# Optimization experiments

Measured on AMD Instinct MI355X. Metric: run time of the kernel, lower is better.

The kernel has to match this reference:

```python
import jax, jax.numpy as jnp
import numpy as np

# Architecture constants (from init_kwargs / Mamba2 defaults)
NL = 4          # num_layer per direction
DM = 256        # d_model (attention_in)
DS = 128        # d_state
DC = 4          # d_conv
DI = 2 * DM     # d_inner = expand * d_model = 512
HD = 64         # headdim
NH = DI // HD   # nheads = 8
NG = 1          # ngroups
D_XBC = DI + 2 * NG * DS           # 768 conv channels
D_INP = 2 * DI + 2 * NG * DS + NH  # 1288 in_proj width
EPS = 1e-5


def rmsnorm(x, w):
    return x * jax.lax.rsqrt(jnp.mean(x * x, axis=-1, keepdims=True) + EPS) * w


def causal_dwconv(x, w, b):
    # x: (B, L, C); w: (C, K); b: (C,) -- causal depthwise conv
    K = w.shape[1]
    L = x.shape[1]
    xp = jnp.pad(x, ((0, 0), (K - 1, 0), (0, 0)))
    y = b
    for k in range(K):  # K=4, fixed small kernel
        y = y + xp[:, k:k + L, :] * w[:, k]
    return y


def ssd_scan(xh, dt, A_log, Bm, Cm):
    # xh: (B,L,H,P), dt: (B,L,H), A_log: (H,), Bm/Cm: (B,L,N) (ngroups=1, broadcast over heads)
    A = -jnp.exp(A_log)                 # (H,)
    decay = jnp.exp(dt * A)             # (B,L,H)
    dtx = dt[..., None] * xh            # (B,L,H,P)
    B, L, H, P = xh.shape
    N = Bm.shape[-1]

    def step(h, inp):
        dec, u, bt, ct = inp            # (B,H), (B,H,P), (B,N), (B,N)
        h = h * dec[..., None, None] + u[..., None] * bt[:, None, None, :]
        y = jnp.einsum('bhpn,bn->bhp', h, ct)
        return h, y

    h0 = jnp.zeros((B, H, P, N), xh.dtype)
    xs = (jnp.moveaxis(decay, 1, 0), jnp.moveaxis(dtx, 1, 0),
          jnp.moveaxis(Bm, 1, 0), jnp.moveaxis(Cm, 1, 0))
    _, ys = jax.lax.scan(step, h0, xs)  # ys: (L,B,H,P)
    return jnp.moveaxis(ys, 0, 1)


def mamba2_mixer(u, Wi, cw, cb, dtb, Al, Dp, gw, Wo):
    B, L, _ = u.shape
    zxbcdt = u @ Wi                                   # (B,L,1288)
    z = zxbcdt[..., :DI]
    xBC = zxbcdt[..., DI:DI + D_XBC]
    dt = zxbcdt[..., DI + D_XBC:]
    xBC = jax.nn.silu(causal_dwconv(xBC, cw, cb))
    xh = xBC[..., :DI].reshape(B, L, NH, HD)
    Bm = xBC[..., DI:DI + NG * DS]
    Cm = xBC[..., DI + NG * DS:]
    dt = jax.nn.softplus(dt + dtb)                    # (B,L,H)
    y = ssd_scan(xh, dt, Al, Bm, Cm) + xh * Dp[None, None, :, None]
    y = y.reshape(B, L, DI)
    g = rmsnorm(y * jax.nn.silu(z), gw)               # RMSNormGated
    return g @ Wo


def run_stack(x, block_ids, nw, Wi, cw, cb, dtb, Al, Dp, gw, Wo):
    res = None
    h = x
    for i in block_ids:
        res = h + res if res is not None else h
        h = mamba2_mixer(rmsnorm(res, nw[i]), Wi[i], cw[i], cb[i],
                         dtb[i], Al[i], Dp[i], gw[i], Wo[i])
    return h + res


def setup_inputs() -> dict:
    key = jax.random.key(0)
    ks = jax.random.split(key, 8)
    B, L = 4, 2048
    NB = 2 * NL  # 8 blocks: forward + backward
    x = jax.random.normal(ks[0], (B, L, DM), jnp.float32)
    nw = jnp.ones((NB, DM), jnp.float32)
    Wi = jax.random.normal(ks[1], (NB, DM, D_INP), jnp.float32) * 0.02
    cw = jax.random.normal(ks[2], (NB, D_XBC, DC), jnp.float32) * 0.2
    cb = jnp.zeros((NB, D_XBC), jnp.float32)
    dt0 = jax.random.uniform(ks[3], (NB, NH), jnp.float32, 0.001, 0.1)
    dtb = dt0 + jnp.log(-jnp.expm1(-dt0))  # inverse softplus
    Al = jnp.log(jax.random.uniform(ks[4], (NB, NH), jnp.float32, 1.0, 16.0))
    Dp = jnp.ones((NB, NH), jnp.float32)
    gw = jnp.ones((NB, DI), jnp.float32)
    Wo = jax.random.normal(ks[5], (NB, DI, DM), jnp.float32) * 0.02
    return {"x": x, "block_norm_w": nw, "in_proj_w": Wi, "conv_w": cw,
            "conv_b": cb, "dt_bias": dtb, "A_log": Al, "D": Dp,
            "gnorm_w": gw, "out_proj_w": Wo}


def reference(x, block_norm_w, in_proj_w, conv_w, conv_b, dt_bias, A_log, D, gnorm_w, out_proj_w):
    fwd = run_stack(x, range(NL), block_norm_w, in_proj_w, conv_w, conv_b,
                    dt_bias, A_log, D, gnorm_w, out_proj_w)
    bwd = run_stack(jnp.flip(x, 1), range(NL, 2 * NL), block_norm_w, in_proj_w,
                    conv_w, conv_b, dt_bias, A_log, D, gnorm_w, out_proj_w)
    return fwd + jnp.flip(bwd, 1)  # bidirectional_merging='add'
```

## Files before the change

### kernel.cpp

```cpp
#include <hip/hip_runtime.h>
#include <hip/hip_bf16.h>
#include <math.h>

#define LSEQ 2048
#define BREAL 4
#define BT 8
#define DM 256
#define DI 512
#define DSZ 128
#define NHEADS 8
#define HDIM 64
#define DXBC 768
#define DINP 1288
#define NINP_PAD 1408
#define NLAYERS 4
#define QCH 64
#define NCH (LSEQ/QCH)
#define CTL 64
#define EPSF 1e-5f

typedef __attribute__((ext_vector_type(8))) short short8b;
typedef __attribute__((ext_vector_type(4))) float f32x4;

__device__ __forceinline__ float siluf(float x){ return x / (1.f + __expf(-x)); }
__device__ __forceinline__ unsigned short f2bf(float x){
    union { float f; unsigned u; } c; c.f = x;
    unsigned r = (c.u + 0x7FFFu + ((c.u >> 16) & 1u)) >> 16;
    return (unsigned short)r;
}
__device__ __forceinline__ float bf2f(unsigned short u){
    union { unsigned u; float f; } c; c.u = ((unsigned)u) << 16;
    return c.f;
}

__global__ __launch_bounds__(256) void k_prep(const float* __restrict__ x, float* __restrict__ res){
    int i = blockIdx.x*256 + threadIdx.x;
    int d4 = i & (DM/4 - 1);
    int t  = i >> 6;
    int l  = t % LSEQ;
    int b  = t / LSEQ;
    const float4* x4 = (const float4*)x;
    float4 v;
    if (b < BREAL) v = x4[((size_t)(b*LSEQ) + l)*(DM/4) + d4];
    else           v = x4[((size_t)((b-BREAL)*LSEQ) + (LSEQ-1-l))*(DM/4) + d4];
    ((float4*)res)[i] = v;
}

__global__ __launch_bounds__(256) void k_wtrans(const float* __restrict__ W, unsigned short* __restrict__ WT,
                                                int K, int N, int Npad){
    __shared__ float sT[32][33];
    int n0 = blockIdx.x*32, k0 = blockIdx.y*32, g = blockIdx.z;
    const float* Wg = W + (size_t)g*K*N;
    unsigned short* WTg = WT + (size_t)g*Npad*K;
    int t = threadIdx.x;
    int r = t >> 3, c4 = (t & 7)*4;
    float4 v;
    if (n0 + c4 + 3 < N) v = *(const float4*)(Wg + (size_t)(k0+r)*N + n0 + c4);
    else {
        float tmp[4];
        #pragma unroll
        for (int j = 0; j < 4; j++) tmp[j] = (n0 + c4 + j < N) ? Wg[(size_t)(k0+r)*N + n0 + c4 + j] : 0.f;
        v = make_float4(tmp[0],tmp[1],tmp[2],tmp[3]);
    }
    sT[c4+0][r] = v.x; sT[c4+1][r] = v.y; sT[c4+2][r] = v.z; sT[c4+3][r] = v.w;
    __syncthreads();
    ushort4 o;
    o.x = f2bf(sT[r][c4+0]); o.y = f2bf(sT[r][c4+1]); o.z = f2bf(sT[r][c4+2]); o.w = f2bf(sT[r][c4+3]);
    *(ushort4*)(WTg + (size_t)(n0+r)*K + k0 + c4) = o;
}

__global__ __launch_bounds__(256) void k_resnorm(const float* __restrict__ res,
                                                 const float* __restrict__ nw, int li,
                                                 unsigned short* __restrict__ u){
    int wid  = (blockIdx.x*256 + threadIdx.x) >> 6;
    int lane = threadIdx.x & 63;
    int b = wid / LSEQ;
    const float* rr = res + (size_t)wid*DM;
    float4 v = ((const float4*)rr)[lane];
    float ss = v.x*v.x + v.y*v.y + v.z*v.z + v.w*v.w;
    #pragma unroll
    for (int o = 32; o >= 1; o >>= 1) ss += __shfl_xor(ss, o, 64);
    float sc = rsqrtf(ss*(1.f/DM) + EPSF);
    int blk = (b < BREAL) ? li : li + NLAYERS;
    float4 w = ((const float4*)(nw + (size_t)blk*DM))[lane];
    ushort4 o4;
    o4.x = f2bf(v.x*sc*w.x); o4.y = f2bf(v.y*sc*w.y); o4.z = f2bf(v.z*sc*w.z); o4.w = f2bf(v.w*sc*w.w);
    *(ushort4*)(u + (size_t)wid*DM + lane*4) = o4;
}

__global__ __launch_bounds__(256) void k_gemm_mfma(const unsigned short* __restrict__ A,
                                                   const unsigned short* __restrict__ WT,
                                                   int K, int N, size_t wt_group_stride, int rows_per_group,
                                                   float* __restrict__ Cf, unsigned short* __restrict__ Cb,
                                                   int mode){
    __shared__ unsigned short sA[128][40];
    __shared__ unsigned short sW[128][40];
    int bn = blockIdx.x, bm = blockIdx.y;
    int row0 = bm*128, n0 = bn*128;
    const unsigned short* WTg = WT + (size_t)(row0 / rows_per_group) * wt_group_stride;
    int t = threadIdx.x;
    int w = t >> 6, lane = t & 63;
    int wr = w >> 1, wc = w & 1;
    int l15 = lane & 15, lg = lane >> 4;
    f32x4 acc[4][4];
    #pragma unroll
    for (int mi = 0; mi < 4; mi++)
        #pragma unroll
        for (int ni = 0; ni < 4; ni++) acc[mi][ni] = (f32x4){0.f,0.f,0.f,0.f};

    int srow = t >> 1, shalf = t & 1;
    const unsigned short* Ap = A + (size_t)(row0 + srow)*K + shalf*16;
    const unsigned short* Wp = WTg + (size_t)(n0 + srow)*K + shalf*16;

    for (int k0 = 0; k0 < K; k0 += 32){
        int4 a0 = *(const int4*)(Ap + k0);
        int4 a1 = *(const int4*)(Ap + k0 + 8);
        int4 w0 = *(const int4*)(Wp + k0);
        int4 w1 = *(const int4*)(Wp + k0 + 8);
        __syncthreads();
        *(int4*)&sA[srow][shalf*16]     = a0;
        *(int4*)&sA[srow][shalf*16 + 8] = a1;
        *(int4*)&sW[srow][shalf*16]     = w0;
        *(int4*)&sW[srow][shalf*16 + 8] = w1;
        __syncthreads();
        short8b af[4], bf[4];
        #pragma unroll
        for (int mi = 0; mi < 4; mi++) af[mi] = *(const short8b*)&sA[wr*64 + mi*16 + l15][lg*8];
        #pragma unroll
        for (int ni = 0; ni < 4; ni++) bf[ni] = *(const short8b*)&sW[wc*64 + ni*16 + l15][lg*8];
        #pragma unroll
        for (int mi = 0; mi < 4; mi++)
            #pragma unroll
            for (int ni = 0; ni < 4; ni++)
                acc[mi][ni] = __builtin_amdgcn_mfma_f32_16x16x32_bf16(af[mi], bf[ni], acc[mi][ni], 0, 0, 0);
    }
    #pragma unroll
    for (int mi = 0; mi < 4; mi++)
        #pragma unroll
        for (int ni = 0; ni < 4; ni++){
            int col = n0 + wc*64 + ni*16 + l15;
            if (col < N){
                #pragma unroll
                for (int r = 0; r < 4; r++){
                    int row = row0 + wr*64 + mi*16 + lg*4 + r;
                    if (mode == 1)      Cb[(size_t)row*N + col] = f2bf(acc[mi][ni][r]);
                    else if (mode == 2) Cf[(size_t)row*N + col] += acc[mi][ni][r];
                    else                Cf[(size_t)row*N + col] = acc[mi][ni][r];
                }
            }
        }
}

__global__ __launch_bounds__(256) void k_conv2(const unsigned short* __restrict__ zxb,
                                               const float* __restrict__ cw, const float* __restrict__ cb,
                                               const float* __restrict__ dtb, const float* __restrict__ Al,
                                               int li, unsigned short* __restrict__ xbcb,
                                               float* __restrict__ dtO, float* __restrict__ laO){
    int bid = blockIdx.x;
    int ch = bid % 3;
    int tl = (bid/3) % (LSEQ/CTL);
    int b  = bid / (3*(LSEQ/CTL));
    int c  = ch*256 + threadIdx.x;
    int blk = (b < BREAL) ? li : li + NLAYERS;
    float4 wv = *(const float4*)(cw + (size_t)blk*DXBC*4 + c*4);
    float bias = cb[(size_t)blk*DXBC + c];
    int l0 = tl*CTL;
    size_t base = ((size_t)b*LSEQ)*DINP + DI + c;
    float xm3 = (l0 >= 3) ? bf2f(zxb[base + (size_t)(l0-3)*DINP]) : 0.f;
    float xm2 = (l0 >= 2) ? bf2f(zxb[base + (size_t)(l0-2)*DINP]) : 0.f;
    float xm1 = (l0 >= 1) ? bf2f(zxb[base + (size_t)(l0-1)*DINP]) : 0.f;
    for (int l = l0; l < l0 + CTL; l++){
        float xv = bf2f(zxb[base + (size_t)l*DINP]);
        float acc = bias + xm3*wv.x + xm2*wv.y + xm1*wv.z + xv*wv.w;
        xbcb[((size_t)(b*LSEQ)+l)*DXBC + c] = f2bf(siluf(acc));
        xm3 = xm2; xm2 = xm1; xm1 = xv;
    }
    if (ch == 0){
        #pragma unroll
        for (int it = 0; it < 2; it++){
            int e = threadIdx.x*2 + it;
            int h = e & 7, dl = e >> 3;
            size_t bl = (size_t)b*LSEQ + l0 + dl;
            float raw = bf2f(zxb[bl*DINP + DI + DXBC + h]) + dtb[blk*NHEADS + h];
            float d = (raw > 20.f) ? raw : log1pf(__expf(raw));
            dtO[bl*NHEADS + h] = d;
            laO[bl*NHEADS + h] = -d*__expf(Al[blk*NHEADS + h]);
        }
    }
}

__global__ __launch_bounds__(256) void k_chunk_state(const unsigned short* __restrict__ xbcb,
                                                     const float* __restrict__ dt, const float* __restrict__ la,
                                                     unsigned short* __restrict__ states, float* __restrict__ decp){
    __shared__ unsigned short sBT[DSZ][72];
    __shared__ unsigned short sXT[HDIM][72];
    __shared__ float sW[4][QCH];
    int bid = blockIdx.x;
    int hg = bid & 1;
    int c  = (bid >> 1) & (NCH-1);
    int b  = bid >> 6;
    int t = threadIdx.x;
    int w = t >> 6, lane = t & 63, l15 = lane & 15, lg = lane >> 4;
    size_t bl0 = (size_t)b*LSEQ + c*QCH;

    {
        int h = hg*4 + w;
        float v = la[(bl0 + lane)*NHEADS + h];
        #pragma unroll
        for (int o = 1; o < 64; o <<= 1){
            float u = __shfl_up(v, o, 64);
            if (lane >= o) v += u;
        }
        float saQ = __shfl(v, 63, 64);
        float dtv = dt[(bl0 + lane)*NHEADS + h];
        sW[w][lane] = dtv * __expf(saQ - v);
        if (lane == 63) decp[((size_t)b*NHEADS + h)*NCH + c] = __expf(v);
    }
    #pragma unroll
    for (int it = 0; it < 4; it++){
        int e = t + 256*it;
        int j = e >> 4, n8 = (e & 15)*8;
        int4 v = *(const int4*)(xbcb + (bl0 + j)*DXBC + DI + n8);
        const unsigned short* pv = (const unsigned short*)&v;
        #pragma unroll
        for (int i = 0; i < 8; i++) sBT[n8+i][j] = pv[i];
    }
    __syncthreads();

    int p0 = (w >> 1)*32, n0 = (w & 1)*64;
    for (int hh = 0; hh < 4; hh++){
        int h = hg*4 + hh;
        #pragma unroll
        for (int it = 0; it < 4; it++){
            int e = t + 256*it;
            int j = e >> 4, p4 = (e & 15)*4;
            ushort4 v = *(const ushort4*)(xbcb + (bl0 + j)*DXBC + h*HDIM + p4);
            float s = sW[hh][j];
            sXT[p4+0][j] = f2bf(bf2f(v.x)*s);
            sXT[p4+1][j] = f2bf(bf2f(v.y)*s);
            sXT[p4+2][j] = f2bf(bf2f(v.z)*s);
            sXT[p4+3][j] = f2bf(bf2f(v.w)*s);
        }
        __syncthreads();
        f32x4 acc[2][4];
        #pragma unroll
        for (int mi = 0; mi < 2; mi++)
            #pragma unroll
            for (int ni = 0; ni < 4; ni++) acc[mi][ni] = (f32x4){0.f,0.f,0.f,0.f};
        #pragma unroll
        for (int kk = 0; kk < 2; kk++){
            short8b a[2], bb[4];
            #pragma unroll
            for (int mi = 0; mi < 2; mi++) a[mi]  = *(const short8b*)&sXT[p0 + mi*16 + l15][kk*32 + lg*8];
            #pragma unroll
            for (int ni = 0; ni < 4; ni++) bb[ni] = *(const short8b*)&sBT[n0 + ni*16 + l15][kk*32 + lg*8];
            #pragma unroll
            for (int mi = 0; mi < 2; mi++)
                #pragma unroll
                for (int ni = 0; ni < 4; ni++)
                    acc[mi][ni] = __builtin_amdgcn_mfma_f32_16x16x32_bf16(a[mi], bb[ni], acc[mi][ni], 0, 0, 0);
        }
        unsigned short* sp = states + (((size_t)b*NHEADS + h)*NCH + c)*(HDIM*DSZ);
        #pragma unroll
        for (int mi = 0; mi < 2; mi++)
            #pragma unroll
            for (int ni = 0; ni < 4; ni++)
                #pragma unroll
                for (int r = 0; r < 4; r++){
                    int p = p0 + mi*16 + lg*4 + r;
                    int n = n0 + ni*16 + l15;
                    sp[(size_t)p*DSZ + n] = f2bf(acc[mi][ni][r]);
                }
        __syncthreads();
    }
}

__global__ __launch_bounds__(256) void k_scan2(unsigned short* __restrict__ states, const float* __restrict__ decp){
    int bh = blockIdx.x >> 3, slice = blockIdx.x & 7;
    int t = threadIdx.x;
    size_t base = (size_t)bh*NCH*(HDIM*DSZ) + slice*1024 + t*4;
    float H0=0.f, H1=0.f, H2=0.f, H3=0.f;
    for (int c = 0; c < NCH; c++){
        float P = decp[bh*NCH + c];
        unsigned short* sp = states + base + (size_t)c*(HDIM*DSZ);
        ushort4 S = *(ushort4*)sp;
        ushort4 Hw;
        Hw.x = f2bf(H0); Hw.y = f2bf(H1); Hw.z = f2bf(H2); Hw.w = f2bf(H3);
        *(ushort4*)sp = Hw;
        H0 = fmaf(H0, P, bf2f(S.x));
        H1 = fmaf(H1, P, bf2f(S.y));
        H2 = fmaf(H2, P, bf2f(S.z));
        H3 = fmaf(H3, P, bf2f(S.w));
    }
}

__global__ __launch_bounds__(256) void k_chunk_y(const unsigned short* __restrict__ xbcb,
                                                 const float* __restrict__ dt, const float* __restrict__ la,
                                                 const unsigned short* __restrict__ states,
                                                 const float* __restrict__ Dp, int li,
                                                 unsigned short* __restrict__ y){
    __shared__ unsigned short sB_[QCH][136];
    __shared__ unsigned short sC_[QCH][136];
    __shared__ unsigned short sS[QCH][72];
    __shared__ unsigned short sXT[HDIM][72];
    __shared__ unsigned short sH[HDIM][136];
    __shared__ float sSa[4][QCH];
    __shared__ float sDt[4][QCH];
    int bid = blockIdx.x;
    int hg = bid & 1;
    int c  = (bid >> 1) & (NCH-1);
    int b  = bid >> 6;
    int blk = (b < BREAL) ? li : li + NLAYERS;
    int t = threadIdx.x;
    int w = t >> 6, lane = t & 63, l15 = lane & 15, lg = lane >> 4;
    size_t bl0 = (size_t)b*LSEQ + c*QCH;

    {
        int h = hg*4 + w;
        float v = la[(bl0 + lane)*NHEADS + h];
        #pragma unroll
        for (int o = 1; o < 64; o <<= 1){
            float u = __shfl_up(v, o, 64);
            if (lane >= o) v += u;
        }
        sSa[w][lane] = v;
        sDt[w][lane] = dt[(bl0 + lane)*NHEADS + h];
    }
    #pragma unroll
    for (int it = 0; it < 4; it++){
        int e = t + 256*it;
        int j = e >> 4, n8 = (e & 15)*8;
        *(int4*)&sB_[j][n8] = *(const int4*)(xbcb + (bl0 + j)*DXBC + DI + n8);
        *(int4*)&sC_[j][n8] = *(const int4*)(xbcb + (bl0 + j)*DXBC + DI + DSZ + n8);
    }
    __syncthreads();

    int i0 = (w >> 1)*32, q0 = (w & 1)*32;

    f32x4 accS[2][2];
    #pragma unroll
    for (int mi = 0; mi < 2; mi++)
        #pragma unroll
        for (int nj = 0; nj < 2; nj++) accS[mi][nj] = (f32x4){0.f,0.f,0.f,0.f};
    #pragma unroll
    for (int kk = 0; kk < 4; kk++){
        short8b a[2], bb[2];
        #pragma unroll
        for (int mi = 0; mi < 2; mi++) a[mi]  = *(const short8b*)&sC_[i0 + mi*16 + l15][kk*32 + lg*8];
        #pragma unroll
        for (int nj = 0; nj < 2; nj++) bb[nj] = *(const short8b*)&sB_[q0 + nj*16 + l15][kk*32 + lg*8];
        #pragma unroll
        for (int mi = 0; mi < 2; mi++)
            #pragma unroll
            for (int nj = 0; nj < 2; nj++)
                accS[mi][nj] = __builtin_amdgcn_mfma_f32_16x16x32_bf16(a[mi], bb[nj], accS[mi][nj], 0, 0, 0);
    }

    for (int hh = 0; hh < 4; hh++){
        int h = hg*4 + hh;
        #pragma unroll
        for (int mi = 0; mi < 2; mi++)
            #pragma unroll
            for (int nj = 0; nj < 2; nj++)
                #pragma unroll
                for (int r = 0; r < 4; r++){
                    int i = i0 + mi*16 + lg*4 + r;
                    int j = q0 + nj*16 + l15;
                    float wgt = (i >= j) ? __expf(sSa[hh][i] - sSa[hh][j]) : 0.f;
                    sS[i][j] = f2bf(accS[mi][nj][r] * wgt);
                }
        #pragma unroll
        for (int it = 0; it < 4; it++){
            int e = t + 256*it;
            int j = e >> 4, p4 = (e & 15)*4;
            ushort4 v = *(const ushort4*)(xbcb + (bl0 + j)*DXBC + h*HDIM + p4);
            float s = sDt[hh][j];
            sXT[p4+0][j] = f2bf(bf2f(v.x)*s);
            sXT[p4+1][j] = f2bf(bf2f(v.y)*s);
            sXT[p4+2][j] = f2bf(bf2f(v.z)*s);
            sXT[p4+3][j] = f2bf(bf2f(v.w)*s);
        }
        {
            size_t sbase = (((size_t)b*NHEADS + h)*NCH + c)*(HDIM*DSZ);
            #pragma unroll
            for (int it = 0; it < 4; it++){
                int e = t + 256*it;
                int p = e >> 4, n8 = (e & 15)*8;
                *(int4*)&sH[p][n8] = *(const int4*)(states + sbase + (size_t)p*DSZ + n8);
            }
        }
        __syncthreads();

        f32x4 accY[2][2], accI[2][2];
        #pragma unroll
        for (int mi = 0; mi < 2; mi++)
            #pragma unroll
            for (int nj = 0; nj < 2; nj++){ accY[mi][nj] = (f32x4){0.f,0.f,0.f,0.f}; accI[mi][nj] = (f32x4){0.f,0.f,0.f,0.f}; }
        #pragma unroll
        for (int kk = 0; kk < 2; kk++){
            short8b a[2], bb[2];
            #pragma unroll
            for (int mi = 0; mi < 2; mi++) a[mi]  = *(const short8b*)&sS[i0 + mi*16 + l15][kk*32 + lg*8];
            #pragma unroll
            for (int nj = 0; nj < 2; nj++) bb[nj] = *(const short8b*)&sXT[q0 + nj*16 + l15][kk*32 + lg*8];
            #pragma unroll
            for (int mi = 0; mi < 2; mi++)
                #pragma unroll
                for (int nj = 0; nj < 2; nj++)
                    accY[mi][nj] = __builtin_amdgcn_mfma_f32_16x16x32_bf16(a[mi], bb[nj], accY[mi][nj], 0, 0, 0);
        }
        #pragma unroll
        for (int kk = 0; kk < 4; kk++){
            short8b a[2], bb[2];
            #pragma unroll
            for (int mi = 0; mi < 2; mi++) a[mi]  = *(const short8b*)&sC_[i0 + mi*16 + l15][kk*32 + lg*8];
            #pragma unroll
            for (int nj = 0; nj < 2; nj++) bb[nj] = *(const short8b*)&sH[q0 + nj*16 + l15][kk*32 + lg*8];
            #pragma unroll
            for (int mi = 0; mi < 2; mi++)
                #pragma unroll
                for (int nj = 0; nj < 2; nj++)
                    accI[mi][nj] = __builtin_amdgcn_mfma_f32_16x16x32_bf16(a[mi], bb[nj], accI[mi][nj], 0, 0, 0);
        }

        float dD = Dp[blk*NHEADS + h];
        #pragma unroll
        for (int mi = 0; mi < 2; mi++)
            #pragma unroll
            for (int r = 0; r < 4; r++){
                int i = i0 + mi*16 + lg*4 + r;
                float ei = __expf(sSa[hh][i]);
                #pragma unroll
                for (int nj = 0; nj < 2; nj++){
                    int p = q0 + nj*16 + l15;
                    float xh = bf2f(xbcb[(bl0 + i)*DXBC + h*HDIM + p]);
                    y[(bl0 + i)*DI + h*HDIM + p] = f2bf(accY[mi][nj][r] + ei*accI[mi][nj][r] + dD*xh);
                }
            }
        __syncthreads();
    }
}

__global__ __launch_bounds__(256) void k_gatenorm(const unsigned short* __restrict__ y, const unsigned short* __restrict__ zxb,
                                                  const float* __restrict__ gw, int li,
                                                  unsigned short* __restrict__ yb){
    int wid  = (blockIdx.x*256 + threadIdx.x) >> 6;
    int lane = threadIdx.x & 63;
    int b = wid / LSEQ;
    int blk = (b < BREAL) ? li : li + NLAYERS;
    const unsigned short* yr = y + (size_t)wid*DI;
    const unsigned short* zr = zxb + (size_t)wid*DINP;
    ushort4 yu0 = *(const ushort4*)(yr + lane*4);
    ushort4 yu1 = *(const ushort4*)(yr + 256 + lane*4);
    ushort4 zu0 = *(const ushort4*)(zr + lane*4);
    ushort4 zu1 = *(const ushort4*)(zr + 256 + lane*4);
    float4 v0, v1;
    v0.x = bf2f(yu0.x)*siluf(bf2f(zu0.x)); v0.y = bf2f(yu0.y)*siluf(bf2f(zu0.y));
    v0.z = bf2f(yu0.z)*siluf(bf2f(zu0.z)); v0.w = bf2f(yu0.w)*siluf(bf2f(zu0.w));
    v1.x = bf2f(yu1.x)*siluf(bf2f(zu1.x)); v1.y = bf2f(yu1.y)*siluf(bf2f(zu1.y));
    v1.z = bf2f(yu1.z)*siluf(bf2f(zu1.z)); v1.w = bf2f(yu1.w)*siluf(bf2f(zu1.w));
    float ss = v0.x*v0.x + v0.y*v0.y + v0.z*v0.z + v0.w*v0.w
             + v1.x*v1.x + v1.y*v1.y + v1.z*v1.z + v1.w*v1.w;
    #pragma unroll
    for (int o = 32; o >= 1; o >>= 1) ss += __shfl_xor(ss, o, 64);
    float sc = rsqrtf(ss*(1.f/DI) + EPSF);
    const float4* w4 = (const float4*)(gw + (size_t)blk*DI);
    float4 w0 = w4[lane], w1 = w4[64 + lane];
    ushort4 o0, o1;
    o0.x = f2bf(v0.x*sc*w0.x); o0.y = f2bf(v0.y*sc*w0.y); o0.z = f2bf(v0.z*sc*w0.z); o0.w = f2bf(v0.w*sc*w0.w);
    o1.x = f2bf(v1.x*sc*w1.x); o1.y = f2bf(v1.y*sc*w1.y); o1.z = f2bf(v1.z*sc*w1.z); o1.w = f2bf(v1.w*sc*w1.w);
    *(ushort4*)(yb + (size_t)wid*DI + lane*4)       = o0;
    *(ushort4*)(yb + (size_t)wid*DI + 256 + lane*4) = o1;
}

__global__ __launch_bounds__(256) void k_final(const float* __restrict__ res, float* __restrict__ out){
    int i = blockIdx.x*256 + threadIdx.x;
    int d4 = i & 63;
    int t  = i >> 6;
    int l = t % LSEQ, b = t / LSEQ;
    size_t fi = ((size_t)(b*LSEQ) + l)*(DM/4) + d4;
    size_t bi = ((size_t)((b+BREAL)*LSEQ) + (LSEQ-1-l))*(DM/4) + d4;
    float4 r1 = ((const float4*)res)[fi];
    float4 r2 = ((const float4*)res)[bi];
    float4 o;
    o.x = r1.x + r2.x;
    o.y = r1.y + r2.y;
    o.z = r1.z + r2.z;
    o.w = r1.w + r2.w;
    ((float4*)out)[i] = o;
}

extern "C" void kernel_launch(void* const* d_in, const int* in_sizes, int n_in,
                              void* d_out, int out_size, void* d_ws, size_t ws_size,
                              hipStream_t stream){
    const float* x   = (const float*)d_in[0];
    const float* nw  = (const float*)d_in[1];
    const float* Wi  = (const float*)d_in[2];
    const float* cw  = (const float*)d_in[3];
    const float* cb  = (const float*)d_in[4];
    const float* dtb = (const float*)d_in[5];
    const float* Al  = (const float*)d_in[6];
    const float* Dp  = (const float*)d_in[7];
    const float* gw  = (const float*)d_in[8];
    const float* Wo  = (const float*)d_in[9];
    float* out = (float*)d_out;

    size_t off = 0;
    auto alloc = [&](size_t bytes){ void* p = (char*)d_ws + off; off += (bytes + 255) & ~(size_t)255; return p; };
    float* RES    = (float*)alloc((size_t)BT*LSEQ*DM*4);
    unsigned short* STATES = (unsigned short*)alloc((size_t)BT*NHEADS*NCH*HDIM*DSZ*2);
    unsigned short* YGB = (unsigned short*)alloc((size_t)BT*LSEQ*DI*2);
    unsigned short* UBUF = YGB;
    unsigned short* ZXB = (unsigned short*)alloc((size_t)BT*LSEQ*DINP*2);
    unsigned short* XBC = (unsigned short*)alloc((size_t)BT*LSEQ*DXBC*2);
    float* DT     = (float*)alloc((size_t)BT*LSEQ*NHEADS*4);
    float* LA     = (float*)alloc((size_t)BT*LSEQ*NHEADS*4);
    unsigned short* YG = (unsigned short*)alloc((size_t)BT*LSEQ*DI*2);
    float* DECP   = (float*)alloc((size_t)BT*NHEADS*NCH*4);
    unsigned short* WiT = (unsigned short*)alloc((size_t)2*NLAYERS*NINP_PAD*DM*2);
    unsigned short* WoT = (unsigned short*)alloc((size_t)2*NLAYERS*DM*DI*2);
    (void)ws_size; (void)in_sizes; (void)n_in; (void)out_size;

    k_prep<<<(BT*LSEQ*DM/4)/256, 256, 0, stream>>>(x, RES);
    k_wtrans<<<dim3(NINP_PAD/32, DM/32, 2*NLAYERS), 256, 0, stream>>>(Wi, WiT, DM, DINP, NINP_PAD);
    k_wtrans<<<dim3(DM/32, DI/32, 2*NLAYERS), 256, 0, stream>>>(Wo, WoT, DI, DM, DM);

    for (int li = 0; li < NLAYERS; li++){
        k_resnorm<<<(BT*LSEQ)/4, 256, 0, stream>>>(RES, nw, li, UBUF);
        k_gemm_mfma<<<dim3(NINP_PAD/128, (BT*LSEQ)/128), 256, 0, stream>>>(
            UBUF, WiT + (size_t)li*NINP_PAD*DM, DM, DINP,
            (size_t)NLAYERS*NINP_PAD*DM, BREAL*LSEQ, nullptr, ZXB, 1);
        k_conv2<<<BT*(LSEQ/CTL)*3, 256, 0, stream>>>(ZXB, cw, cb, dtb, Al, li, XBC, DT, LA);
        k_chunk_state<<<BT*NCH*2, 256, 0, stream>>>(XBC, DT, LA, STATES, DECP);
        k_scan2<<<BT*NHEADS*8, 256, 0, stream>>>(STATES, DECP);
        k_chunk_y<<<BT*NCH*2, 256, 0, stream>>>(XBC, DT, LA, STATES, Dp, li, YG);
        k_gatenorm<<<(BT*LSEQ)/4, 256, 0, stream>>>(YG, ZXB, gw, li, YGB);
        k_gemm_mfma<<<dim3(DM/128, (BT*LSEQ)/128), 256, 0, stream>>>(
            YGB, WoT + (size_t)li*DM*DI, DI, DM,
            (size_t)NLAYERS*DM*DI, BREAL*LSEQ, RES, nullptr, 2);
    }
    k_final<<<(BREAL*LSEQ*DM/4)/256, 256, 0, stream>>>(RES, out);
}
```

Before: 704.0 us.

## Add dedicated 128x256 in_proj GEMM kernel with K=64 tiles and XCD-aware block remap

Replaces the generic 128x128 MFMA GEMM for in_proj with a new 512-thread kernel that computes 128x256 output tiles with a K step of 64. Block IDs are remapped so consecutive tiles land on the same XCD for better L2 reuse. The weight padding grows from 1408 to 1536 so N divides 256, which adds some wasted columns. The out_proj kernel's LDS row stride also changes from 40 to 42, likely to reduce bank conflicts.

```diff
diff --git a/kernel.cpp b/kernel.cpp
--- a/kernel.cpp
+++ b/kernel.cpp
@@ -12,7 +12,7 @@
 #define HDIM 64
 #define DXBC 768
 #define DINP 1288
-#define NINP_PAD 1408
+#define NINP_PAD 1536
 #define NLAYERS 4
 #define QCH 64
 #define NCH (LSEQ/QCH)
@@ -88,13 +88,91 @@
     *(ushort4*)(u + (size_t)wid*DM + lane*4) = o4;
 }
 
+__global__ __launch_bounds__(512) void k_gemm_in(const unsigned short* __restrict__ A,
+                                                 const unsigned short* __restrict__ WT,
+                                                 int K, int N, size_t wt_group_stride, int rows_per_group,
+                                                 unsigned short* __restrict__ Cb){
+    __shared__ unsigned short sA[128][68];
+    __shared__ unsigned short sW[256][68];
+    int nwg = gridDim.x*gridDim.y;
+    int bid = blockIdx.y*gridDim.x + blockIdx.x;
+    int q = nwg >> 3, rm = nwg & 7;
+    int xcd = bid & 7, local = bid >> 3;
+    int nid = (xcd < rm ? xcd*(q+1) : rm*(q+1) + (xcd-rm)*q) + local;
+    int bn = nid % gridDim.x;
+    int bm = nid / gridDim.x;
+    int row0 = bm*128, n0 = bn*256;
+    const unsigned short* WTg = WT + (size_t)(row0 / rows_per_group) * wt_group_stride;
+    int t = threadIdx.x;
+    int w = t >> 6, lane = t & 63;
+    int wr = w >> 2, wc = w & 3;
+    int l15 = lane & 15, lg = lane >> 4;
+    f32x4 acc[4][4];
+    #pragma unroll
+    for (int mi = 0; mi < 4; mi++)
+        #pragma unroll
+        for (int ni = 0; ni < 4; ni++) acc[mi][ni] = (f32x4){0.f,0.f,0.f,0.f};
+
+    for (int k0 = 0; k0 < K; k0 += 64){
+        int4 av[2], wv[4];
+        #pragma unroll
+        for (int i = 0; i < 2; i++){
+            int e = t + 512*i;
+            av[i] = *(const int4*)(A + (size_t)(row0 + (e>>3))*K + k0 + (e&7)*8);
+        }
+        #pragma unroll
+        for (int i = 0; i < 4; i++){
+            int e = t + 512*i;
+            wv[i] = *(const int4*)(WTg + (size_t)(n0 + (e>>3))*K + k0 + (e&7)*8);
+        }
+        __syncthreads();
+        #pragma unroll
+        for (int i = 0; i < 2; i++){
+            int e = t + 512*i;
+            *(int4*)&sA[e>>3][(e&7)*8] = av[i];
+        }
+        #pragma unroll
+        for (int i = 0; i < 4; i++){
+            int e = t + 512*i;
+            *(int4*)&sW[e>>3][(e&7)*8] = wv[i];
+        }
+        __syncthreads();
+        #pragma unroll
+        for (int kk = 0; kk < 2; kk++){
+            short8b af[4], bf[4];
+            #pragma unroll
+            for (int mi = 0; mi < 4; mi++) af[mi] = *(const short8b*)&sA[wr*64 + mi*16 + l15][kk*32 + lg*8];
+            #pragma unroll
+            for (int ni = 0; ni < 4; ni++) bf[ni] = *(const short8b*)&sW[wc*64 + ni*16 + l15][kk*32 + lg*8];
+            #pragma unroll
+            for (int mi = 0; mi < 4; mi++)
+                #pragma unroll
+                for (int ni = 0; ni < 4; ni++)
+                    acc[mi][ni] = __builtin_amdgcn_mfma_f32_16x16x32_bf16(af[mi], bf[ni], acc[mi][ni], 0, 0, 0);
+        }
+    }
+    #pragma unroll
+    for (int mi = 0; mi < 4; mi++)
+        #pragma unroll
+        for (int ni = 0; ni < 4; ni++){
+            int col = n0 + wc*64 + ni*16 + l15;
+            if (col < N){
+                #pragma unroll
+                for (int r = 0; r < 4; r++){
+                    int row = row0 + wr*64 + mi*16 + lg*4 + r;
+                    Cb[(size_t)row*N + col] = f2bf(acc[mi][ni][r]);
+                }
+            }
+        }
+}
+
 __global__ __launch_bounds__(256) void k_gemm_mfma(const unsigned short* __restrict__ A,
                                                    const unsigned short* __restrict__ WT,
                                                    int K, int N, size_t wt_group_stride, int rows_per_group,
                                                    float* __restrict__ Cf, unsigned short* __restrict__ Cb,
                                                    int mode){
-    __shared__ unsigned short sA[128][40];
-    __shared__ unsigned short sW[128][40];
+    __shared__ unsigned short sA[128][42];
+    __shared__ unsigned short sW[128][42];
     int bn = blockIdx.x, bm = blockIdx.y;
     int row0 = bm*128, n0 = bn*128;
     const unsigned short* WTg = WT + (size_t)(row0 / rows_per_group) * wt_group_stride;
@@ -527,9 +605,9 @@
 
     for (int li = 0; li < NLAYERS; li++){
         k_resnorm<<<(BT*LSEQ)/4, 256, 0, stream>>>(RES, nw, li, UBUF);
-        k_gemm_mfma<<<dim3(NINP_PAD/128, (BT*LSEQ)/128), 256, 0, stream>>>(
+        k_gemm_in<<<dim3(NINP_PAD/256, (BT*LSEQ)/128), 512, 0, stream>>>(
             UBUF, WiT + (size_t)li*NINP_PAD*DM, DM, DINP,
-            (size_t)NLAYERS*NINP_PAD*DM, BREAL*LSEQ, nullptr, ZXB, 1);
+            (size_t)NLAYERS*NINP_PAD*DM, BREAL*LSEQ, ZXB);
         k_conv2<<<BT*(LSEQ/CTL)*3, 256, 0, stream>>>(ZXB, cw, cb, dtb, Al, li, XBC, DT, LA);
         k_chunk_state<<<BT*NCH*2, 256, 0, stream>>>(XBC, DT, LA, STATES, DECP);
         k_scan2<<<BT*NHEADS*8, 256, 0, stream>>>(STATES, DECP);
```

Result: slower. 786.9 us (+11.8%).
